# Kernel tuning notes

Measured on AMD Instinct MI355X. Metric: run time of the kernel, lower is better.

## Reference

```python
import jax, jax.numpy as jnp
import numpy as np

C_S, C_P, FEAT_DIM, NUM_BINS = 256, 128, 64, 22
TOTAL_EDGE_FEATS = FEAT_DIM * 2 + NUM_BINS * 2 + 2  # embed_diffuse_mask=True
LN_EPS = 1e-5


def calc_distogram(pos, min_bin, max_bin, num_bins):
    # pos: [B, N, 3] -> one-hot distance bins [B, N, N, num_bins]
    d = jnp.linalg.norm(pos[:, :, None, :] - pos[:, None, :, :], axis=-1)[..., None]
    lower = jnp.linspace(min_bin, max_bin, num_bins, dtype=pos.dtype)
    upper = jnp.concatenate([lower[1:], jnp.array([1e8], dtype=pos.dtype)])
    return ((d > lower) & (d < upper)).astype(pos.dtype)


def cross_concat(f):
    # f: [B, N, D] -> [B, N, N, 2D]: row-broadcast feats then col-broadcast feats
    B, N, D = f.shape
    fi = jnp.broadcast_to(f[:, :, None, :], (B, N, N, D))
    fj = jnp.broadcast_to(f[:, None, :, :], (B, N, N, D))
    return jnp.concatenate([fi, fj], axis=-1)


def setup_inputs() -> dict:
    key = jax.random.key(0)
    ks = jax.random.split(key, 12)
    B, N = 2, 512
    inp = {
        'init_node_embed': jax.random.normal(ks[0], (B, N, C_S), jnp.float32),
        'trans_t': jax.random.normal(ks[1], (B, N, 3), jnp.float32),
        'trans_sc': jax.random.normal(ks[2], (B, N, 3), jnp.float32),
        'edge_mask': jnp.ones((B, N, N), jnp.float32),
        'diffuse_mask': jnp.ones((B, N), jnp.float32),
        # params (fan-in scaled)
        'Wsp': jax.random.normal(ks[3], (C_S, FEAT_DIM), jnp.float32) / np.sqrt(C_S),
        'bsp': jnp.zeros((FEAT_DIM,), jnp.float32),
        'W1': jax.random.normal(ks[4], (TOTAL_EDGE_FEATS, C_P), jnp.float32) / np.sqrt(TOTAL_EDGE_FEATS),
        'b1': jnp.zeros((C_P,), jnp.float32),
        'W2': jax.random.normal(ks[5], (C_P, C_P), jnp.float32) / np.sqrt(C_P),
        'b2': jnp.zeros((C_P,), jnp.float32),
        'W3': jax.random.normal(ks[6], (C_P, C_P), jnp.float32) / np.sqrt(C_P),
        'b3': jnp.zeros((C_P,), jnp.float32),
        'ln_g': jnp.ones((C_P,), jnp.float32),
        'ln_b': jnp.zeros((C_P,), jnp.float32),
    }
    return inp


def reference(init_node_embed, trans_t, trans_sc, edge_mask, diffuse_mask,
              Wsp, bsp, W1, b1, W2, b2, W3, b3, ln_g, ln_b):
    p_i = init_node_embed @ Wsp + bsp                      # [B,N,feat_dim]
    cross_node = cross_concat(p_i)                          # [B,N,N,2*feat_dim]
    dist_feats = calc_distogram(trans_t, 1e-3, 20.0, NUM_BINS)
    sc_feats = calc_distogram(trans_sc, 1e-3, 20.0, NUM_BINS)
    diff_feat = cross_concat(diffuse_mask[..., None])       # [B,N,N,2]
    feats = jnp.concatenate([cross_node, dist_feats, sc_feats, diff_feat], axis=-1)
    h = jax.nn.relu(feats @ W1 + b1)
    h = jax.nn.relu(h @ W2 + b2)
    h = h @ W3 + b3
    mu = jnp.mean(h, axis=-1, keepdims=True)
    var = jnp.mean(jnp.square(h - mu), axis=-1, keepdims=True)
    h = (h - mu) * jax.lax.rsqrt(var + LN_EPS) * ln_g + ln_b
    return h * edge_mask[..., None]
```

## Files before the change

### kernel.cpp

```cpp
#include <hip/hip_runtime.h>
#include <math.h>

#define NB 2
#define NN 512
#define CS 256
#define CP 128
#define FD 64
#define NBINS 22
#define EPB 64

typedef __attribute__((ext_vector_type(8))) short bf16x8;
typedef __attribute__((ext_vector_type(4))) short bf16x4;
typedef __attribute__((ext_vector_type(4))) float f32x4;

__device__ __forceinline__ unsigned short f2bf_rne(float x) {
    unsigned int u = __float_as_uint(x);
    unsigned int r = (u + 0x7fffu + ((u >> 16) & 1u)) >> 16;
    return (unsigned short)r;
}
__device__ __forceinline__ float bf2f(unsigned short b) {
    return __uint_as_float(((unsigned int)b) << 16);
}

__device__ __forceinline__ int bin_of(float d, float step) {
    const float fk = __fdiv_rn(__fsub_rn(d, 0.001f), step);
    int k0 = (int)fk;
    k0 = k0 < 1 ? 1 : (k0 > 20 ? 20 : k0);
    int row = -1;
    #pragma unroll
    for (int dk = -1; dk <= 1; ++dk) {
        const int k = k0 + dk;
        const float lo = __fadd_rn(0.001f, __fmul_rn((float)k, step));
        const float hi = (k == NBINS - 1)
                       ? 1e8f
                       : __fadd_rn(0.001f, __fmul_rn((float)(k + 1), step));
        row = (d > lo && d < hi) ? k : row;
    }
    return row;
}

__global__ __launch_bounds__(256) void ef_prep_kernel(
    const float* __restrict__ x,
    const float* __restrict__ diffuse,
    const float* __restrict__ Wsp,
    const float* __restrict__ bsp,
    const float* __restrict__ W1,
    const float* __restrict__ b1,
    const float* __restrict__ W2,
    const float* __restrict__ W3,
    float* __restrict__ qr,
    unsigned short* __restrict__ Wp)
{
    __shared__ float xs[CS];
    __shared__ float ps[FD];
    const int t = threadIdx.x;
    if (blockIdx.x < 1024) {
        const int n = blockIdx.x;
        xs[t] = x[(size_t)n * CS + t];
        __syncthreads();
        if (t < FD) {
            float acc = bsp[t];
            #pragma unroll 8
            for (int k = 0; k < CS; ++k)
                acc = fmaf(xs[k], Wsp[k * FD + t], acc);
            ps[t] = acc;
        }
        __syncthreads();
        const float dm = diffuse[n];
        const int c = t & (CP - 1);
        if (t < CP) {
            float acc = b1[c] + dm * W1[172 * CP + c];
            #pragma unroll 8
            for (int k = 0; k < FD; ++k)
                acc = fmaf(ps[k], W1[k * CP + c], acc);
            qr[(size_t)n * CP + c] = acc;
        } else {
            float acc = dm * W1[173 * CP + c];
            #pragma unroll 8
            for (int k = 0; k < FD; ++k)
                acc = fmaf(ps[k], W1[(FD + k) * CP + c], acc);
            qr[(size_t)(1024 + n) * CP + c] = acc;
        }
    } else {
        const int s = (blockIdx.x - 1024) * 256 + t;
        const int j    = s & 7;
        const int lane = (s >> 3) & 63;
        const int mt   = (s >> 9) & 7;
        const int ki   = s >> 12;
        const int k = 32 * ki + 8 * (lane >> 4) + j;
        const int n = 16 * mt + (lane & 15);
        const float w2 = W2[k * CP + n];
        const float w3 = W3[k * CP + n];
        const unsigned short h2 = f2bf_rne(w2);
        const unsigned short l2 = f2bf_rne(w2 - bf2f(h2));
        const unsigned short h3 = f2bf_rne(w3);
        const unsigned short l3 = f2bf_rne(w3 - bf2f(h3));
        Wp[s]         = h2;
        Wp[16384 + s] = l2;
        Wp[32768 + s] = h3;
        Wp[49152 + s] = l3;
    }
}

__global__ __launch_bounds__(256, 4) void ef_edge_kernel(
    const float* __restrict__ trans_t,
    const float* __restrict__ trans_sc,
    const float* __restrict__ edge_mask,
    const float* __restrict__ W1,
    const float* __restrict__ b2,
    const float* __restrict__ b3,
    const float* __restrict__ ln_g,
    const float* __restrict__ ln_b,
    const float* __restrict__ qr,
    const unsigned short* __restrict__ Wp,
    float* __restrict__ out)
{
    __shared__ unsigned short hb[16384];
    char* hb8 = (char*)hb;

    const int t   = threadIdx.x;
    const int blk = blockIdx.x;
    const int jt  = blk & 7;
    const int i   = (blk >> 3) & (NN - 1);
    const int b   = blk >> 12;
    const int j0  = jt * EPB;
    const int nodeI  = b * NN + i;
    const int nodeJ0 = b * NN + j0;

    const int w  = t >> 6;
    const int l  = t & 63;
    const int lr = l & 15;
    const int lg = l >> 4;

    bf16x8 w2h[4][2];
    #pragma unroll
    for (int ki = 0; ki < 4; ++ki)
        #pragma unroll
        for (int mt = 0; mt < 2; ++mt)
            w2h[ki][mt] = *(const bf16x8*)(Wp + (((size_t)ki * 8 + (2 * w + mt)) * 64 + l) * 8);

    const int e1 = t >> 2;
    const int c0 = (t & 3) * 32;
    const int nj = nodeJ0 + e1;
    const float step = __fdiv_rn(__fsub_rn(20.0f, 0.001f), 21.0f);
    const float ix0 = trans_t[nodeI * 3 + 0], ix1 = trans_t[nodeI * 3 + 1], ix2 = trans_t[nodeI * 3 + 2];
    const float jx0 = trans_t[nj * 3 + 0],    jx1 = trans_t[nj * 3 + 1],    jx2 = trans_t[nj * 3 + 2];
    const float iy0 = trans_sc[nodeI * 3 + 0], iy1 = trans_sc[nodeI * 3 + 1], iy2 = trans_sc[nodeI * 3 + 2];
    const float jy0 = trans_sc[nj * 3 + 0],    jy1 = trans_sc[nj * 3 + 1],    jy2 = trans_sc[nj * 3 + 2];
    float dx = __fsub_rn(ix0, jx0), dy = __fsub_rn(ix1, jx1), dz = __fsub_rn(ix2, jx2);
    const float dT = sqrtf(__fadd_rn(__fadd_rn(__fmul_rn(dx, dx), __fmul_rn(dy, dy)), __fmul_rn(dz, dz)));
    dx = __fsub_rn(iy0, jy0); dy = __fsub_rn(iy1, jy1); dz = __fsub_rn(iy2, jy2);
    const float dS = sqrtf(__fadd_rn(__fadd_rn(__fmul_rn(dx, dx), __fmul_rn(dy, dy)), __fmul_rn(dz, dz)));
    const int kT = bin_of(dT, step);
    const int kS = bin_of(dS, step);

    {
        const float fT = (kT < 0) ? 0.0f : 1.0f;
        const float fS = (kS < 0) ? 0.0f : 1.0f;
        const float* qrow = qr + (size_t)nodeI * CP + c0;
        const float* rrow = qr + (size_t)(1024 + nj) * CP + c0;
        const float* wTr  = W1 + (size_t)(kT < 0 ? 0 : 128 + kT) * CP + c0;
        const float* wSr  = W1 + (size_t)(kS < 0 ? 0 : 150 + kS) * CP + c0;
        #pragma unroll
        for (int ch = 0; ch < 4; ++ch) {
            const int cc = ch * 8;
            const float4 qa = *(const float4*)(qrow + cc);
            const float4 qb = *(const float4*)(qrow + cc + 4);
            const float4 ra = *(const float4*)(rrow + cc);
            const float4 rb = *(const float4*)(rrow + cc + 4);
            const float4 ta = *(const float4*)(wTr + cc);
            const float4 tb = *(const float4*)(wTr + cc + 4);
            const float4 sa = *(const float4*)(wSr + cc);
            const float4 sb = *(const float4*)(wSr + cc + 4);
            float h[8];
            h[0] = fmaxf(qa.x + ra.x + fT * ta.x + fS * sa.x, 0.0f);
            h[1] = fmaxf(qa.y + ra.y + fT * ta.y + fS * sa.y, 0.0f);
            h[2] = fmaxf(qa.z + ra.z + fT * ta.z + fS * sa.z, 0.0f);
            h[3] = fmaxf(qa.w + ra.w + fT * ta.w + fS * sa.w, 0.0f);
            h[4] = fmaxf(qb.x + rb.x + fT * tb.x + fS * sb.x, 0.0f);
            h[5] = fmaxf(qb.y + rb.y + fT * tb.y + fS * sb.y, 0.0f);
            h[6] = fmaxf(qb.z + rb.z + fT * tb.z + fS * sb.z, 0.0f);
            h[7] = fmaxf(qb.w + rb.w + fT * tb.w + fS * sb.w, 0.0f);
            bf16x8 H, L;
            #pragma unroll
            for (int u = 0; u < 8; ++u) {
                const unsigned short hi = f2bf_rne(h[u]);
                H[u] = (short)hi;
                L[u] = (short)f2bf_rne(h[u] - bf2f(hi));
            }
            const unsigned int ad = (unsigned int)e1 * 256 +
                (((unsigned int)(2 * (c0 + cc))) ^ (((unsigned int)e1 & 7) << 4));
            *(bf16x8*)(hb8 + ad) = H;
            *(bf16x8*)(hb8 + 16384 + ad) = L;
        }
    }

    bf16x8 w2l[4][2];
    #pragma unroll
    for (int ki = 0; ki < 4; ++ki)
        #pragma unroll
        for (int mt = 0; mt < 2; ++mt)
            w2l[ki][mt] = *(const bf16x8*)(Wp + 16384 + (((size_t)ki * 8 + (2 * w + mt)) * 64 + l) * 8);
    __syncthreads();

    f32x4 acc[2][4];
    #pragma unroll
    for (int mt = 0; mt < 2; ++mt) {
        const float4 bv = *(const float4*)&b2[16 * (2 * w + mt) + 4 * lg];
        #pragma unroll
        for (int nt = 0; nt < 4; ++nt) {
            acc[mt][nt][0] = bv.x; acc[mt][nt][1] = bv.y;
            acc[mt][nt][2] = bv.z; acc[mt][nt][3] = bv.w;
        }
    }
    #pragma unroll
    for (int ki = 0; ki < 4; ++ki) {
        bf16x8 bh[4], bl[4];
        #pragma unroll
        for (int nt = 0; nt < 4; ++nt) {
            const int e = 16 * nt + lr;
            const unsigned int ad = (unsigned int)e * 256 +
                (((unsigned int)(64 * ki + 16 * lg)) ^ (((unsigned int)e & 7) << 4));
            bh[nt] = *(const bf16x8*)(hb8 + ad);
            bl[nt] = *(const bf16x8*)(hb8 + 16384 + ad);
        }
        __builtin_amdgcn_s_setprio(1);
        #pragma unroll
        for (int mt = 0; mt < 2; ++mt)
            #pragma unroll
            for (int nt = 0; nt < 4; ++nt) {
                acc[mt][nt] = __builtin_amdgcn_mfma_f32_16x16x32_bf16(w2h[ki][mt], bh[nt], acc[mt][nt], 0, 0, 0);
                acc[mt][nt] = __builtin_amdgcn_mfma_f32_16x16x32_bf16(w2l[ki][mt], bh[nt], acc[mt][nt], 0, 0, 0);
                acc[mt][nt] = __builtin_amdgcn_mfma_f32_16x16x32_bf16(w2h[ki][mt], bl[nt], acc[mt][nt], 0, 0, 0);
            }
        __builtin_amdgcn_s_setprio(0);
    }

    bf16x8 w3h[4][2];
    #pragma unroll
    for (int ki = 0; ki < 4; ++ki)
        #pragma unroll
        for (int mt = 0; mt < 2; ++mt)
            w3h[ki][mt] = *(const bf16x8*)(Wp + 32768 + (((size_t)ki * 8 + (2 * w + mt)) * 64 + l) * 8);
    __syncthreads();

    #pragma unroll
    for (int mt = 0; mt < 2; ++mt) {
        const int mtg = 2 * w + mt;
        #pragma unroll
        for (int nt = 0; nt < 4; ++nt) {
            const int e = 16 * nt + lr;
            float v[4];
            v[0] = fmaxf(acc[mt][nt][0], 0.0f);
            v[1] = fmaxf(acc[mt][nt][1], 0.0f);
            v[2] = fmaxf(acc[mt][nt][2], 0.0f);
            v[3] = fmaxf(acc[mt][nt][3], 0.0f);
            bf16x4 H, L;
            #pragma unroll
            for (int u = 0; u < 4; ++u) {
                const unsigned short hi = f2bf_rne(v[u]);
                H[u] = (short)hi;
                L[u] = (short)f2bf_rne(v[u] - bf2f(hi));
            }
            const unsigned int ad = (unsigned int)e * 256 +
                (((unsigned int)(32 * mtg + 8 * lg)) ^ (((unsigned int)e & 7) << 4));
            *(bf16x4*)(hb8 + ad) = H;
            *(bf16x4*)(hb8 + 16384 + ad) = L;
        }
    }

    bf16x8 w3l[4][2];
    #pragma unroll
    for (int ki = 0; ki < 4; ++ki)
        #pragma unroll
        for (int mt = 0; mt < 2; ++mt)
            w3l[ki][mt] = *(const bf16x8*)(Wp + 49152 + (((size_t)ki * 8 + (2 * w + mt)) * 64 + l) * 8);
    __syncthreads();

    f32x4 acc3[2][4];
    #pragma unroll
    for (int mt = 0; mt < 2; ++mt) {
        const float4 bv = *(const float4*)&b3[16 * (2 * w + mt) + 4 * lg];
        #pragma unroll
        for (int nt = 0; nt < 4; ++nt) {
            acc3[mt][nt][0] = bv.x; acc3[mt][nt][1] = bv.y;
            acc3[mt][nt][2] = bv.z; acc3[mt][nt][3] = bv.w;
        }
    }
    #pragma unroll
    for (int ki = 0; ki < 4; ++ki) {
        bf16x8 bh[4], bl[4];
        #pragma unroll
        for (int nt = 0; nt < 4; ++nt) {
            const int e = 16 * nt + lr;
            const unsigned int ad = (unsigned int)e * 256 +
                (((unsigned int)(64 * ki + 16 * lg)) ^ (((unsigned int)e & 7) << 4));
            bh[nt] = *(const bf16x8*)(hb8 + ad);
            bl[nt] = *(const bf16x8*)(hb8 + 16384 + ad);
        }
        __builtin_amdgcn_s_setprio(1);
        #pragma unroll
        for (int mt = 0; mt < 2; ++mt)
            #pragma unroll
            for (int nt = 0; nt < 4; ++nt) {
                acc3[mt][nt] = __builtin_amdgcn_mfma_f32_16x16x32_bf16(w3h[ki][mt], bh[nt], acc3[mt][nt], 0, 0, 0);
                acc3[mt][nt] = __builtin_amdgcn_mfma_f32_16x16x32_bf16(w3l[ki][mt], bh[nt], acc3[mt][nt], 0, 0, 0);
                acc3[mt][nt] = __builtin_amdgcn_mfma_f32_16x16x32_bf16(w3h[ki][mt], bl[nt], acc3[mt][nt], 0, 0, 0);
            }
        __builtin_amdgcn_s_setprio(0);
    }
    __syncthreads();

    float* psum_s  = (float*)hb8;
    float* pqsum_s = (float*)(hb8 + 4352);
    float* mus     = (float*)(hb8 + 8704);
    float* invs    = (float*)(hb8 + 8960);
    #pragma unroll
    for (int nt = 0; nt < 4; ++nt) {
        const int e = 16 * nt + lr;
        float s = 0.0f, s2 = 0.0f;
        #pragma unroll
        for (int mt = 0; mt < 2; ++mt)
            #pragma unroll
            for (int r = 0; r < 4; ++r) {
                const float v = acc3[mt][nt][r];
                s += v;
                s2 = fmaf(v, v, s2);
            }
        psum_s[e * 17 + 4 * w + lg]  = s;
        pqsum_s[e * 17 + 4 * w + lg] = s2;
    }
    __syncthreads();

    {
        const int e = t & 63;
        float s = 0.0f, s2 = 0.0f;
        #pragma unroll
        for (int k = 0; k < 16; ++k) {
            s  += psum_s[e * 17 + k];
            s2 += pqsum_s[e * 17 + k];
        }
        const float mu  = s * (1.0f / 128.0f);
        const float var = s2 * (1.0f / 128.0f) - mu * mu;
        mus[e]  = mu;
        invs[e] = rsqrtf(var + 1e-5f);
    }
    __syncthreads();

    {
        float4 g4[2], bb4[2];
        #pragma unroll
        for (int mt = 0; mt < 2; ++mt) {
            const int n0 = 16 * (2 * w + mt) + 4 * lg;
            g4[mt]  = *(const float4*)&ln_g[n0];
            bb4[mt] = *(const float4*)&ln_b[n0];
        }
        #pragma unroll
        for (int nt = 0; nt < 4; ++nt) {
            const int e = 16 * nt + lr;
            const size_t erow = ((size_t)(b * NN + i)) * NN + (j0 + e);
            const float em  = edge_mask[erow];
            const float mu  = mus[e];
            const float inv = invs[e];
            float* op = out + erow * CP;
            #pragma unroll
            for (int mt = 0; mt < 2; ++mt) {
                const int n0 = 16 * (2 * w + mt) + 4 * lg;
                float4 o;
                o.x = ((acc3[mt][nt][0] - mu) * inv * g4[mt].x + bb4[mt].x) * em;
                o.y = ((acc3[mt][nt][1] - mu) * inv * g4[mt].y + bb4[mt].y) * em;
                o.z = ((acc3[mt][nt][2] - mu) * inv * g4[mt].z + bb4[mt].z) * em;
                o.w = ((acc3[mt][nt][3] - mu) * inv * g4[mt].w + bb4[mt].w) * em;
                *(float4*)(op + n0) = o;
            }
        }
    }
}

extern "C" void kernel_launch(void* const* d_in, const int* in_sizes, int n_in,
                              void* d_out, int out_size, void* d_ws, size_t ws_size,
                              hipStream_t stream) {
    const float* init_node = (const float*)d_in[0];
    const float* trans_t   = (const float*)d_in[1];
    const float* trans_sc  = (const float*)d_in[2];
    const float* edge_mask = (const float*)d_in[3];
    const float* diffuse   = (const float*)d_in[4];
    const float* Wsp       = (const float*)d_in[5];
    const float* bsp       = (const float*)d_in[6];
    const float* W1        = (const float*)d_in[7];
    const float* b1        = (const float*)d_in[8];
    const float* W2        = (const float*)d_in[9];
    const float* b2        = (const float*)d_in[10];
    const float* W3        = (const float*)d_in[11];
    const float* b3        = (const float*)d_in[12];
    const float* ln_g      = (const float*)d_in[13];
    const float* ln_b      = (const float*)d_in[14];
    float* out = (float*)d_out;
    float* qr  = (float*)d_ws;
    unsigned short* Wp = (unsigned short*)((char*)d_ws + (1 << 20));

    ef_prep_kernel<<<1024 + 64, 256, 0, stream>>>(
        init_node, diffuse, Wsp, bsp, W1, b1, W2, W3, qr, Wp);
    ef_edge_kernel<<<NB * NN * (NN / EPB), 256, 0, stream>>>(
        trans_t, trans_sc, edge_mask, W1, b2, b3, ln_g, ln_b, qr, Wp, out);
}
```

Measured before the change: 222.6 us.

## Loop over j-tiles per block and restage LayerNorm through shared memory

```diff
diff --git a/kernel.cpp b/kernel.cpp
--- a/kernel.cpp
+++ b/kernel.cpp
@@ -1,4 +1,5 @@
 #include <hip/hip_runtime.h>
+#include <hip/hip_bf16.h>
 #include <math.h>
 
 #define NB 2
@@ -20,6 +21,12 @@
 }
 __device__ __forceinline__ float bf2f(unsigned short b) {
     return __uint_as_float(((unsigned int)b) << 16);
+}
+__device__ __forceinline__ unsigned short f2bf(float x) {
+    __hip_bfloat16 h = __float2bfloat16(x);
+    unsigned short u;
+    __builtin_memcpy(&u, &h, 2);
+    return u;
 }
 
 __device__ __forceinline__ int bin_of(float d, float step) {
@@ -37,6 +44,11 @@
         row = (d > lo && d < hi) ? k : row;
     }
     return row;
+}
+
+__device__ __forceinline__ unsigned int swz512(int e, int boff) {
+    return (unsigned int)e * 512 +
+           (unsigned int)(boff ^ ((e & 7) << 4) ^ (((boff >> 7) & 3) << 4));
 }
 
 __global__ __launch_bounds__(256) void ef_prep_kernel(
@@ -120,17 +132,16 @@
 
     const int t   = threadIdx.x;
     const int blk = blockIdx.x;
-    const int jt  = blk & 7;
-    const int i   = (blk >> 3) & (NN - 1);
-    const int b   = blk >> 12;
-    const int j0  = jt * EPB;
-    const int nodeI  = b * NN + i;
-    const int nodeJ0 = b * NN + j0;
+    const int i   = blk & (NN - 1);
+    const int b   = blk >> 9;
+    const int nodeI = b * NN + i;
 
     const int w  = t >> 6;
     const int l  = t & 63;
     const int lr = l & 15;
     const int lg = l >> 4;
+    const int e1 = t >> 2;
+    const int c0 = (t & 3) * 32;
 
     bf16x8 w2h[4][2];
     #pragma unroll
@@ -139,241 +150,235 @@
         for (int mt = 0; mt < 2; ++mt)
             w2h[ki][mt] = *(const bf16x8*)(Wp + (((size_t)ki * 8 + (2 * w + mt)) * 64 + l) * 8);
 
-    const int e1 = t >> 2;
-    const int c0 = (t & 3) * 32;
-    const int nj = nodeJ0 + e1;
     const float step = __fdiv_rn(__fsub_rn(20.0f, 0.001f), 21.0f);
     const float ix0 = trans_t[nodeI * 3 + 0], ix1 = trans_t[nodeI * 3 + 1], ix2 = trans_t[nodeI * 3 + 2];
-    const float jx0 = trans_t[nj * 3 + 0],    jx1 = trans_t[nj * 3 + 1],    jx2 = trans_t[nj * 3 + 2];
     const float iy0 = trans_sc[nodeI * 3 + 0], iy1 = trans_sc[nodeI * 3 + 1], iy2 = trans_sc[nodeI * 3 + 2];
-    const float jy0 = trans_sc[nj * 3 + 0],    jy1 = trans_sc[nj * 3 + 1],    jy2 = trans_sc[nj * 3 + 2];
-    float dx = __fsub_rn(ix0, jx0), dy = __fsub_rn(ix1, jx1), dz = __fsub_rn(ix2, jx2);
-    const float dT = sqrtf(__fadd_rn(__fadd_rn(__fmul_rn(dx, dx), __fmul_rn(dy, dy)), __fmul_rn(dz, dz)));
-    dx = __fsub_rn(iy0, jy0); dy = __fsub_rn(iy1, jy1); dz = __fsub_rn(iy2, jy2);
-    const float dS = sqrtf(__fadd_rn(__fadd_rn(__fmul_rn(dx, dx), __fmul_rn(dy, dy)), __fmul_rn(dz, dz)));
-    const int kT = bin_of(dT, step);
-    const int kS = bin_of(dS, step);
-
-    {
-        const float fT = (kT < 0) ? 0.0f : 1.0f;
-        const float fS = (kS < 0) ? 0.0f : 1.0f;
-        const float* qrow = qr + (size_t)nodeI * CP + c0;
-        const float* rrow = qr + (size_t)(1024 + nj) * CP + c0;
-        const float* wTr  = W1 + (size_t)(kT < 0 ? 0 : 128 + kT) * CP + c0;
-        const float* wSr  = W1 + (size_t)(kS < 0 ? 0 : 150 + kS) * CP + c0;
-        #pragma unroll
-        for (int ch = 0; ch < 4; ++ch) {
-            const int cc = ch * 8;
-            const float4 qa = *(const float4*)(qrow + cc);
-            const float4 qb = *(const float4*)(qrow + cc + 4);
-            const float4 ra = *(const float4*)(rrow + cc);
-            const float4 rb = *(const float4*)(rrow + cc + 4);
-            const float4 ta = *(const float4*)(wTr + cc);
-            const float4 tb = *(const float4*)(wTr + cc + 4);
-            const float4 sa = *(const float4*)(wSr + cc);
-            const float4 sb = *(const float4*)(wSr + cc + 4);
-            float h[8];
-            h[0] = fmaxf(qa.x + ra.x + fT * ta.x + fS * sa.x, 0.0f);
-            h[1] = fmaxf(qa.y + ra.y + fT * ta.y + fS * sa.y, 0.0f);
-            h[2] = fmaxf(qa.z + ra.z + fT * ta.z + fS * sa.z, 0.0f);
-            h[3] = fmaxf(qa.w + ra.w + fT * ta.w + fS * sa.w, 0.0f);
-            h[4] = fmaxf(qb.x + rb.x + fT * tb.x + fS * sb.x, 0.0f);
-            h[5] = fmaxf(qb.y + rb.y + fT * tb.y + fS * sb.y, 0.0f);
-            h[6] = fmaxf(qb.z + rb.z + fT * tb.z + fS * sb.z, 0.0f);
-            h[7] = fmaxf(qb.w + rb.w + fT * tb.w + fS * sb.w, 0.0f);
-            bf16x8 H, L;
-            #pragma unroll
-            for (int u = 0; u < 8; ++u) {
-                const unsigned short hi = f2bf_rne(h[u]);
-                H[u] = (short)hi;
-                L[u] = (short)f2bf_rne(h[u] - bf2f(hi));
-            }
-            const unsigned int ad = (unsigned int)e1 * 256 +
-                (((unsigned int)(2 * (c0 + cc))) ^ (((unsigned int)e1 & 7) << 4));
-            *(bf16x8*)(hb8 + ad) = H;
-            *(bf16x8*)(hb8 + 16384 + ad) = L;
-        }
-    }
-
-    bf16x8 w2l[4][2];
-    #pragma unroll
-    for (int ki = 0; ki < 4; ++ki)
-        #pragma unroll
-        for (int mt = 0; mt < 2; ++mt)
-            w2l[ki][mt] = *(const bf16x8*)(Wp + 16384 + (((size_t)ki * 8 + (2 * w + mt)) * 64 + l) * 8);
-    __syncthreads();
-
-    f32x4 acc[2][4];
-    #pragma unroll
-    for (int mt = 0; mt < 2; ++mt) {
-        const float4 bv = *(const float4*)&b2[16 * (2 * w + mt) + 4 * lg];
-        #pragma unroll
-        for (int nt = 0; nt < 4; ++nt) {
-            acc[mt][nt][0] = bv.x; acc[mt][nt][1] = bv.y;
-            acc[mt][nt][2] = bv.z; acc[mt][nt][3] = bv.w;
-        }
-    }
-    #pragma unroll
-    for (int ki = 0; ki < 4; ++ki) {
-        bf16x8 bh[4], bl[4];
-        #pragma unroll
-        for (int nt = 0; nt < 4; ++nt) {
-            const int e = 16 * nt + lr;
-            const unsigned int ad = (unsigned int)e * 256 +
-                (((unsigned int)(64 * ki + 16 * lg)) ^ (((unsigned int)e & 7) << 4));
-            bh[nt] = *(const bf16x8*)(hb8 + ad);
-            bl[nt] = *(const bf16x8*)(hb8 + 16384 + ad);
-        }
-        __builtin_amdgcn_s_setprio(1);
-        #pragma unroll
-        for (int mt = 0; mt < 2; ++mt)
-            #pragma unroll
-            for (int nt = 0; nt < 4; ++nt) {
-                acc[mt][nt] = __builtin_amdgcn_mfma_f32_16x16x32_bf16(w2h[ki][mt], bh[nt], acc[mt][nt], 0, 0, 0);
-                acc[mt][nt] = __builtin_amdgcn_mfma_f32_16x16x32_bf16(w2l[ki][mt], bh[nt], acc[mt][nt], 0, 0, 0);
-                acc[mt][nt] = __builtin_amdgcn_mfma_f32_16x16x32_bf16(w2h[ki][mt], bl[nt], acc[mt][nt], 0, 0, 0);
-            }
-        __builtin_amdgcn_s_setprio(0);
-    }
-
-    bf16x8 w3h[4][2];
-    #pragma unroll
-    for (int ki = 0; ki < 4; ++ki)
-        #pragma unroll
-        for (int mt = 0; mt < 2; ++mt)
-            w3h[ki][mt] = *(const bf16x8*)(Wp + 32768 + (((size_t)ki * 8 + (2 * w + mt)) * 64 + l) * 8);
-    __syncthreads();
-
-    #pragma unroll
-    for (int mt = 0; mt < 2; ++mt) {
-        const int mtg = 2 * w + mt;
-        #pragma unroll
-        for (int nt = 0; nt < 4; ++nt) {
-            const int e = 16 * nt + lr;
-            float v[4];
-            v[0] = fmaxf(acc[mt][nt][0], 0.0f);
-            v[1] = fmaxf(acc[mt][nt][1], 0.0f);
-            v[2] = fmaxf(acc[mt][nt][2], 0.0f);
-            v[3] = fmaxf(acc[mt][nt][3], 0.0f);
-            bf16x4 H, L;
-            #pragma unroll
-            for (int u = 0; u < 4; ++u) {
-                const unsigned short hi = f2bf_rne(v[u]);
-                H[u] = (short)hi;
-                L[u] = (short)f2bf_rne(v[u] - bf2f(hi));
-            }
-            const unsigned int ad = (unsigned int)e * 256 +
-                (((unsigned int)(32 * mtg + 8 * lg)) ^ (((unsigned int)e & 7) << 4));
-            *(bf16x4*)(hb8 + ad) = H;
-            *(bf16x4*)(hb8 + 16384 + ad) = L;
-        }
-    }
-
-    bf16x8 w3l[4][2];
-    #pragma unroll
-    for (int ki = 0; ki < 4; ++ki)
-        #pragma unroll
-        for (int mt = 0; mt < 2; ++mt)
-            w3l[ki][mt] = *(const bf16x8*)(Wp + 49152 + (((size_t)ki * 8 + (2 * w + mt)) * 64 + l) * 8);
-    __syncthreads();
-
-    f32x4 acc3[2][4];
-    #pragma unroll
-    for (int mt = 0; mt < 2; ++mt) {
-        const float4 bv = *(const float4*)&b3[16 * (2 * w + mt) + 4 * lg];
-        #pragma unroll
-        for (int nt = 0; nt < 4; ++nt) {
-            acc3[mt][nt][0] = bv.x; acc3[mt][nt][1] = bv.y;
-            acc3[mt][nt][2] = bv.z; acc3[mt][nt][3] = bv.w;
-        }
-    }
-    #pragma unroll
-    for (int ki = 0; ki < 4; ++ki) {
-        bf16x8 bh[4], bl[4];
-        #pragma unroll
-        for (int nt = 0; nt < 4; ++nt) {
-            const int e = 16 * nt + lr;
-            const unsigned int ad = (unsigned int)e * 256 +
-                (((unsigned int)(64 * ki + 16 * lg)) ^ (((unsigned int)e & 7) << 4));
-            bh[nt] = *(const bf16x8*)(hb8 + ad);
-            bl[nt] = *(const bf16x8*)(hb8 + 16384 + ad);
-        }
-        __builtin_amdgcn_s_setprio(1);
-        #pragma unroll
-        for (int mt = 0; mt < 2; ++mt)
-            #pragma unroll
-            for (int nt = 0; nt < 4; ++nt) {
-                acc3[mt][nt] = __builtin_amdgcn_mfma_f32_16x16x32_bf16(w3h[ki][mt], bh[nt], acc3[mt][nt], 0, 0, 0);
-                acc3[mt][nt] = __builtin_amdgcn_mfma_f32_16x16x32_bf16(w3l[ki][mt], bh[nt], acc3[mt][nt], 0, 0, 0);
-                acc3[mt][nt] = __builtin_amdgcn_mfma_f32_16x16x32_bf16(w3h[ki][mt], bl[nt], acc3[mt][nt], 0, 0, 0);
-            }
-        __builtin_amdgcn_s_setprio(0);
-    }
-    __syncthreads();
-
-    float* psum_s  = (float*)hb8;
-    float* pqsum_s = (float*)(hb8 + 4352);
-    float* mus     = (float*)(hb8 + 8704);
-    float* invs    = (float*)(hb8 + 8960);
-    #pragma unroll
-    for (int nt = 0; nt < 4; ++nt) {
-        const int e = 16 * nt + lr;
-        float s = 0.0f, s2 = 0.0f;
-        #pragma unroll
-        for (int mt = 0; mt < 2; ++mt)
-            #pragma unroll
-            for (int r = 0; r < 4; ++r) {
-                const float v = acc3[mt][nt][r];
-                s += v;
-                s2 = fmaf(v, v, s2);
-            }
-        psum_s[e * 17 + 4 * w + lg]  = s;
-        pqsum_s[e * 17 + 4 * w + lg] = s2;
-    }
-    __syncthreads();
-
-    {
-        const int e = t & 63;
-        float s = 0.0f, s2 = 0.0f;
-        #pragma unroll
-        for (int k = 0; k < 16; ++k) {
-            s  += psum_s[e * 17 + k];
-            s2 += pqsum_s[e * 17 + k];
-        }
-        const float mu  = s * (1.0f / 128.0f);
-        const float var = s2 * (1.0f / 128.0f) - mu * mu;
-        mus[e]  = mu;
-        invs[e] = rsqrtf(var + 1e-5f);
-    }
-    __syncthreads();
-
-    {
-        float4 g4[2], bb4[2];
+    const float* qrow = qr + (size_t)nodeI * CP + c0;
+
+    #pragma unroll 1
+    for (int jt = 0; jt < 8; ++jt) {
+        const int j0 = jt * EPB;
+        const int nj = b * NN + j0 + e1;
+
+        float dx = __fsub_rn(ix0, trans_t[nj * 3 + 0]);
+        float dy = __fsub_rn(ix1, trans_t[nj * 3 + 1]);
+        float dz = __fsub_rn(ix2, trans_t[nj * 3 + 2]);
+        const float dT = sqrtf(__fadd_rn(__fadd_rn(__fmul_rn(dx, dx), __fmul_rn(dy, dy)), __fmul_rn(dz, dz)));
+        dx = __fsub_rn(iy0, trans_sc[nj * 3 + 0]);
+        dy = __fsub_rn(iy1, trans_sc[nj * 3 + 1]);
+        dz = __fsub_rn(iy2, trans_sc[nj * 3 + 2]);
+        const float dS = sqrtf(__fadd_rn(__fadd_rn(__fmul_rn(dx, dx), __fmul_rn(dy, dy)), __fmul_rn(dz, dz)));
+        const int kT = bin_of(dT, step);
+        const int kS = bin_of(dS, step);
+
+        {
+            const float fT = (kT < 0) ? 0.0f : 1.0f;
+            const float fS = (kS < 0) ? 0.0f : 1.0f;
+            const float* rrow = qr + (size_t)(1024 + nj) * CP + c0;
+            const float* wTr  = W1 + (size_t)(kT < 0 ? 0 : 128 + kT) * CP + c0;
+            const float* wSr  = W1 + (size_t)(kS < 0 ? 0 : 150 + kS) * CP + c0;
+            #pragma unroll
+            for (int ch = 0; ch < 4; ++ch) {
+                const int cc = ch * 8;
+                const float4 qa = *(const float4*)(qrow + cc);
+                const float4 qb = *(const float4*)(qrow + cc + 4);
+                const float4 ra = *(const float4*)(rrow + cc);
+                const float4 rb = *(const float4*)(rrow + cc + 4);
+                const float4 ta = *(const float4*)(wTr + cc);
+                const float4 tb = *(const float4*)(wTr + cc + 4);
+                const float4 sa = *(const float4*)(wSr + cc);
+                const float4 sb = *(const float4*)(wSr + cc + 4);
+                float h[8];
+                h[0] = fmaxf(qa.x + ra.x + fT * ta.x + fS * sa.x, 0.0f);
+                h[1] = fmaxf(qa.y + ra.y + fT * ta.y + fS * sa.y, 0.0f);
+                h[2] = fmaxf(qa.z + ra.z + fT * ta.z + fS * sa.z, 0.0f);
+                h[3] = fmaxf(qa.w + ra.w + fT * ta.w + fS * sa.w, 0.0f);
+                h[4] = fmaxf(qb.x + rb.x + fT * tb.x + fS * sb.x, 0.0f);
+                h[5] = fmaxf(qb.y + rb.y + fT * tb.y + fS * sb.y, 0.0f);
+                h[6] = fmaxf(qb.z + rb.z + fT * tb.z + fS * sb.z, 0.0f);
+                h[7] = fmaxf(qb.w + rb.w + fT * tb.w + fS * sb.w, 0.0f);
+                bf16x8 H, L;
+                #pragma unroll
+                for (int u = 0; u < 8; ++u) {
+                    const unsigned short hi = f2bf(h[u]);
+                    H[u] = (short)hi;
+                    L[u] = (short)f2bf(h[u] - bf2f(hi));
+                }
+                const unsigned int ad = (unsigned int)e1 * 256 +
+                    (((unsigned int)(2 * (c0 + cc))) ^ (((unsigned int)e1 & 7) << 4));
+                *(bf16x8*)(hb8 + ad) = H;
+                *(bf16x8*)(hb8 + 16384 + ad) = L;
+            }
+        }
+
+        bf16x8 w2l[4][2];
+        #pragma unroll
+        for (int ki = 0; ki < 4; ++ki)
+            #pragma unroll
+            for (int mt = 0; mt < 2; ++mt)
+                w2l[ki][mt] = *(const bf16x8*)(Wp + 16384 + (((size_t)ki * 8 + (2 * w + mt)) * 64 + l) * 8);
+        __syncthreads();
+
+        f32x4 acc[2][4];
         #pragma unroll
         for (int mt = 0; mt < 2; ++mt) {
-            const int n0 = 16 * (2 * w + mt) + 4 * lg;
-            g4[mt]  = *(const float4*)&ln_g[n0];
-            bb4[mt] = *(const float4*)&ln_b[n0];
-        }
-        #pragma unroll
-        for (int nt = 0; nt < 4; ++nt) {
-            const int e = 16 * nt + lr;
+            const float4 bv = *(const float4*)&b2[16 * (2 * w + mt) + 4 * lg];
+            #pragma unroll
+            for (int nt = 0; nt < 4; ++nt) {
+                acc[mt][nt][0] = bv.x; acc[mt][nt][1] = bv.y;
+                acc[mt][nt][2] = bv.z; acc[mt][nt][3] = bv.w;
+            }
+        }
+        #pragma unroll
+        for (int ki = 0; ki < 4; ++ki) {
+            bf16x8 bh[4], bl[4];
+            #pragma unroll
+            for (int nt = 0; nt < 4; ++nt) {
+                const int e = 16 * nt + lr;
+                const unsigned int ad = (unsigned int)e * 256 +
+                    (((unsigned int)(64 * ki + 16 * lg)) ^ (((unsigned int)e & 7) << 4));
+                bh[nt] = *(const bf16x8*)(hb8 + ad);
+                bl[nt] = *(const bf16x8*)(hb8 + 16384 + ad);
+            }
+            __builtin_amdgcn_s_setprio(1);
+            #pragma unroll
+            for (int mt = 0; mt < 2; ++mt)
+                #pragma unroll
+                for (int nt = 0; nt < 4; ++nt) {
+                    acc[mt][nt] = __builtin_amdgcn_mfma_f32_16x16x32_bf16(w2h[ki][mt], bh[nt], acc[mt][nt], 0, 0, 0);
+                    acc[mt][nt] = __builtin_amdgcn_mfma_f32_16x16x32_bf16(w2l[ki][mt], bh[nt], acc[mt][nt], 0, 0, 0);
+                    acc[mt][nt] = __builtin_amdgcn_mfma_f32_16x16x32_bf16(w2h[ki][mt], bl[nt], acc[mt][nt], 0, 0, 0);
+                }
+            __builtin_amdgcn_s_setprio(0);
+        }
+
+        bf16x8 w3h[4][2];
+        #pragma unroll
+        for (int ki = 0; ki < 4; ++ki)
+            #pragma unroll
+            for (int mt = 0; mt < 2; ++mt)
+                w3h[ki][mt] = *(const bf16x8*)(Wp + 32768 + (((size_t)ki * 8 + (2 * w + mt)) * 64 + l) * 8);
+        __syncthreads();
+
+        #pragma unroll
+        for (int mt = 0; mt < 2; ++mt) {
+            const int mtg = 2 * w + mt;
+            #pragma unroll
+            for (int nt = 0; nt < 4; ++nt) {
+                const int e = 16 * nt + lr;
+                float v[4];
+                v[0] = fmaxf(acc[mt][nt][0], 0.0f);
+                v[1] = fmaxf(acc[mt][nt][1], 0.0f);
+                v[2] = fmaxf(acc[mt][nt][2], 0.0f);
+                v[3] = fmaxf(acc[mt][nt][3], 0.0f);
+                bf16x4 H, L;
+                #pragma unroll
+                for (int u = 0; u < 4; ++u) {
+                    const unsigned short hi = f2bf(v[u]);
+                    H[u] = (short)hi;
+                    L[u] = (short)f2bf(v[u] - bf2f(hi));
+                }
+                const unsigned int ad = (unsigned int)e * 256 +
+                    (((unsigned int)(32 * mtg + 8 * lg)) ^ (((unsigned int)e & 7) << 4));
+                *(bf16x4*)(hb8 + ad) = H;
+                *(bf16x4*)(hb8 + 16384 + ad) = L;
+            }
+        }
+
+        bf16x8 w3l[4][2];
+        #pragma unroll
+        for (int ki = 0; ki < 4; ++ki)
+            #pragma unroll
+            for (int mt = 0; mt < 2; ++mt)
+                w3l[ki][mt] = *(const bf16x8*)(Wp + 49152 + (((size_t)ki * 8 + (2 * w + mt)) * 64 + l) * 8);
+        __syncthreads();
+
+        f32x4 acc3[2][4];
+        #pragma unroll
+        for (int mt = 0; mt < 2; ++mt) {
+            const float4 bv = *(const float4*)&b3[16 * (2 * w + mt) + 4 * lg];
+            #pragma unroll
+            for (int nt = 0; nt < 4; ++nt) {
+                acc3[mt][nt][0] = bv.x; acc3[mt][nt][1] = bv.y;
+                acc3[mt][nt][2] = bv.z; acc3[mt][nt][3] = bv.w;
+            }
+        }
+        #pragma unroll
+        for (int ki = 0; ki < 4; ++ki) {
+            bf16x8 bh[4], bl[4];
+            #pragma unroll
+            for (int nt = 0; nt < 4; ++nt) {
+                const int e = 16 * nt + lr;
+                const unsigned int ad = (unsigned int)e * 256 +
+                    (((unsigned int)(64 * ki + 16 * lg)) ^ (((unsigned int)e & 7) << 4));
+                bh[nt] = *(const bf16x8*)(hb8 + ad);
+                bl[nt] = *(const bf16x8*)(hb8 + 16384 + ad);
+            }
+            __builtin_amdgcn_s_setprio(1);
+            #pragma unroll
+            for (int mt = 0; mt < 2; ++mt)
+                #pragma unroll
+                for (int nt = 0; nt < 4; ++nt) {
+                    acc3[mt][nt] = __builtin_amdgcn_mfma_f32_16x16x32_bf16(w3h[ki][mt], bh[nt], acc3[mt][nt], 0, 0, 0);
+                    acc3[mt][nt] = __builtin_amdgcn_mfma_f32_16x16x32_bf16(w3l[ki][mt], bh[nt], acc3[mt][nt], 0, 0, 0);
+                    acc3[mt][nt] = __builtin_amdgcn_mfma_f32_16x16x32_bf16(w3h[ki][mt], bl[nt], acc3[mt][nt], 0, 0, 0);
+                }
+            __builtin_amdgcn_s_setprio(0);
+        }
+        __syncthreads();
+
+        #pragma unroll
+        for (int mt = 0; mt < 2; ++mt) {
+            const int mtg = 2 * w + mt;
+            #pragma unroll
+            for (int nt = 0; nt < 4; ++nt) {
+                const int e = 16 * nt + lr;
+                float4 vv;
+                vv.x = acc3[mt][nt][0]; vv.y = acc3[mt][nt][1];
+                vv.z = acc3[mt][nt][2]; vv.w = acc3[mt][nt][3];
+                *(float4*)(hb8 + swz512(e, 64 * mtg + 16 * lg)) = vv;
+            }
+        }
+        __syncthreads();
+
+        {
+            const int e = e1;
+            float vals[32];
+            float s = 0.0f;
+            #pragma unroll
+            for (int cc = 0; cc < 32; cc += 4) {
+                const float4 v = *(const float4*)(hb8 + swz512(e, 4 * (c0 + cc)));
+                vals[cc] = v.x; vals[cc + 1] = v.y; vals[cc + 2] = v.z; vals[cc + 3] = v.w;
+                s += v.x + v.y + v.z + v.w;
+            }
+            s += __shfl_xor(s, 1);
+            s += __shfl_xor(s, 2);
+            const float mu = s * (1.0f / 128.0f);
+            float s2 = 0.0f;
+            #pragma unroll
+            for (int cc = 0; cc < 32; ++cc) {
+                const float d = vals[cc] - mu;
+                s2 = fmaf(d, d, s2);
+            }
+            s2 += __shfl_xor(s2, 1);
+            s2 += __shfl_xor(s2, 2);
+            const float inv = rsqrtf(s2 * (1.0f / 128.0f) + 1e-5f);
             const size_t erow = ((size_t)(b * NN + i)) * NN + (j0 + e);
-            const float em  = edge_mask[erow];
-            const float mu  = mus[e];
-            const float inv = invs[e];
-            float* op = out + erow * CP;
-            #pragma unroll
-            for (int mt = 0; mt < 2; ++mt) {
-                const int n0 = 16 * (2 * w + mt) + 4 * lg;
-                float4 o;
-                o.x = ((acc3[mt][nt][0] - mu) * inv * g4[mt].x + bb4[mt].x) * em;
-                o.y = ((acc3[mt][nt][1] - mu) * inv * g4[mt].y + bb4[mt].y) * em;
-                o.z = ((acc3[mt][nt][2] - mu) * inv * g4[mt].z + bb4[mt].z) * em;
-                o.w = ((acc3[mt][nt][3] - mu) * inv * g4[mt].w + bb4[mt].w) * em;
-                *(float4*)(op + n0) = o;
-            }
-        }
+            const float em = edge_mask[erow];
+            float* op = out + erow * CP + c0;
+            #pragma unroll
+            for (int cc = 0; cc < 32; cc += 4) {
+                const float4 g  = *(const float4*)&ln_g[c0 + cc];
+                const float4 be = *(const float4*)&ln_b[c0 + cc];
+                float4 o4;
+                o4.x = ((vals[cc + 0] - mu) * inv * g.x + be.x) * em;
+                o4.y = ((vals[cc + 1] - mu) * inv * g.y + be.y) * em;
+                o4.z = ((vals[cc + 2] - mu) * inv * g.z + be.z) * em;
+                o4.w = ((vals[cc + 3] - mu) * inv * g.w + be.w) * em;
+                *(float4*)&op[cc] = o4;
+            }
+        }
+        __syncthreads();
     }
 }
 
@@ -401,6 +406,6 @@
 
     ef_prep_kernel<<<1024 + 64, 256, 0, stream>>>(
         init_node, diffuse, Wsp, bsp, W1, b1, W2, W3, qr, Wp);
-    ef_edge_kernel<<<NB * NN * (NN / EPB), 256, 0, stream>>>(
+    ef_edge_kernel<<<NB * NN, 256, 0, stream>>>(
         trans_t, trans_sc, edge_mask, W1, b2, b3, ln_g, ln_b, qr, Wp, out);
 }
```

After: 643.5 us. 189% more time.
